# Kernel tuning notes

Measured on AMD Instinct MI355X. Metric: run time of the kernel, lower is better.

Reference implementation:

```python
import jax, jax.numpy as jnp
import numpy as np

D_MODEL = 1024
NUM_HEADS = 16
D_K = D_MODEL // NUM_HEADS


def setup_inputs() -> dict:
    key = jax.random.key(0)
    ks = jax.random.split(key, 11)
    B, S = 4, 2048
    s = 1.0 / np.sqrt(D_MODEL)
    return {
        "query": jax.random.normal(ks[0], (B, S, D_MODEL), jnp.float32),
        "key": jax.random.normal(ks[1], (B, S, D_MODEL), jnp.float32),
        "value": jax.random.normal(ks[2], (B, S, D_MODEL), jnp.float32),
        "Wq": jax.random.normal(ks[3], (D_MODEL, D_MODEL), jnp.float32) * s,
        "bq": jnp.zeros((D_MODEL,), jnp.float32),
        "Wk": jax.random.normal(ks[4], (D_MODEL, D_MODEL), jnp.float32) * s,
        "bk": jnp.zeros((D_MODEL,), jnp.float32),
        "Wv": jax.random.normal(ks[5], (D_MODEL, D_MODEL), jnp.float32) * s,
        "bv": jnp.zeros((D_MODEL,), jnp.float32),
        "Wo": jax.random.normal(ks[6], (D_MODEL, D_MODEL), jnp.float32) * s,
        "bo": jnp.zeros((D_MODEL,), jnp.float32),
    }


def reference(query, key, value, Wq, bq, Wk, bk, Wv, bv, Wo, bo):
    B, Sq, _ = query.shape
    Sk = key.shape[1]
    # linear projections (torch Linear: x @ W.T + b)
    q = query @ Wq.T + bq
    k = key @ Wk.T + bk
    v = value @ Wv.T + bv
    # [B, H, S, d_k]
    q = q.reshape(B, Sq, NUM_HEADS, D_K).transpose(0, 2, 1, 3)
    k = k.reshape(B, Sk, NUM_HEADS, D_K).transpose(0, 2, 1, 3)
    v = v.reshape(B, Sk, NUM_HEADS, D_K).transpose(0, 2, 1, 3)
    scores = jnp.einsum("bhqd,bhkd->bhqk", q, k) / jnp.sqrt(jnp.float32(D_K)).astype(q.dtype)
    attn = jax.nn.softmax(scores, axis=-1)
    out = jnp.einsum("bhqk,bhkd->bhqd", attn, v)
    out = out.transpose(0, 2, 1, 3).reshape(B, Sq, D_MODEL)
    return out @ Wo.T + bo
```

## Files before the change

kernel.cpp:

```cpp
#include <hip/hip_runtime.h>
#include <hip/hip_bf16.h>
#include <cstdint>
#include <cstddef>

typedef __attribute__((ext_vector_type(8))) short bf16x8;
typedef __attribute__((ext_vector_type(4))) short bf16x4;
typedef __attribute__((ext_vector_type(4))) float f32x4;
typedef __attribute__((ext_vector_type(2))) unsigned int u32x2;

#define NH 16
#define DK 64
#define SEQ 2048
#define DM 1024
#define QSCALE 0.18033688011112042f

__device__ __forceinline__ short f2bf(float f) {
    union { float f; unsigned u; } x; x.f = f;
    unsigned r = x.u + 0x7fffu + ((x.u >> 16) & 1u);
    return (short)(r >> 16);
}

__device__ __forceinline__ unsigned pk2(float a, float b) {
    union { float f; unsigned u; } x, y; x.f = a; y.f = b;
    return __builtin_amdgcn_perm(y.u + 0x8000u, x.u + 0x8000u, 0x07060302u);
}

__device__ __forceinline__ void glds16(const short* g, short* l) {
    __builtin_amdgcn_global_load_lds((const __attribute__((address_space(1))) unsigned int*)g,
                                     (__attribute__((address_space(3))) unsigned int*)l, 16, 0, 0);
}

__global__ __launch_bounds__(256)
void cvt_all(const float* __restrict__ xq, const float* __restrict__ xk, const float* __restrict__ xv,
             const float* __restrict__ Wq, const float* __restrict__ Wk,
             const float* __restrict__ Wv, const float* __restrict__ Wo,
             short* __restrict__ xb0, short* __restrict__ xb1, short* __restrict__ xb2,
             short* __restrict__ Wb)
{
    const int bid = blockIdx.x;
    const float* src;
    short* dst;
    float sc = 1.0f;
    int i;
    if (bid < 12288) {
        int z = bid >> 12;
        src = (z == 0) ? xq : (z == 1) ? xk : xv;
        dst = (z == 0) ? xb0 : (z == 1) ? xb1 : xb2;
        i = (bid & 4095) * 2048 + threadIdx.x * 8;
    } else {
        int wb = bid - 12288;
        int z = wb >> 9;
        src = (z == 0) ? Wq : (z == 1) ? Wk : (z == 2) ? Wv : Wo;
        dst = Wb + (size_t)z * DM * DM;
        sc = (z == 0) ? QSCALE : 1.0f;
        i = (wb & 511) * 2048 + threadIdx.x * 8;
    }
    float4 a = *(const float4*)&src[i];
    float4 b = *(const float4*)&src[i + 4];
    bf16x8 o = { f2bf(a.x * sc), f2bf(a.y * sc), f2bf(a.z * sc), f2bf(a.w * sc),
                 f2bf(b.x * sc), f2bf(b.y * sc), f2bf(b.z * sc), f2bf(b.w * sc) };
    *(bf16x8*)&dst[i] = o;
}

__global__ __launch_bounds__(256)
void cvt_x(const float* __restrict__ src, short* __restrict__ dst)
{
    int i = (blockIdx.x * 256 + threadIdx.x) * 8;
    float4 a = *(const float4*)&src[i];
    float4 b = *(const float4*)&src[i + 4];
    bf16x8 o = { f2bf(a.x), f2bf(a.y), f2bf(a.z), f2bf(a.w),
                 f2bf(b.x), f2bf(b.y), f2bf(b.z), f2bf(b.w) };
    *(bf16x8*)&dst[i] = o;
}

__global__ __launch_bounds__(256)
void cvt_w(const float* __restrict__ Wq, const float* __restrict__ Wk,
           const float* __restrict__ Wv, const float* __restrict__ Wo,
           short* __restrict__ dst)
{
    int z = blockIdx.y;
    const float* s = (z == 0) ? Wq : (z == 1) ? Wk : (z == 2) ? Wv : Wo;
    float sc = (z == 0) ? QSCALE : 1.0f;
    int i = (blockIdx.x * 256 + threadIdx.x) * 8;
    float4 a = *(const float4*)&s[i];
    float4 b = *(const float4*)&s[i + 4];
    bf16x8 o = { f2bf(a.x * sc), f2bf(a.y * sc), f2bf(a.z * sc), f2bf(a.w * sc),
                 f2bf(b.x * sc), f2bf(b.y * sc), f2bf(b.z * sc), f2bf(b.w * sc) };
    *(bf16x8*)&dst[(size_t)z * DM * DM + i] = o;
}

#define GEMM_CORE(P0, OFF0, P1, OFF1)                                                      \
    __shared__ short As[128 * 32];                                                         \
    __shared__ short Bs[128 * 32];                                                         \
    f32x4 acc[4][4] = {};                                                                  \
    const int t = threadIdx.x;                                                             \
    const int lane = t & 63;                                                               \
    const int w = t >> 6;                                                                  \
    const int wm = (w >> 1) * 64, wn = (w & 1) * 64;                                       \
    const int l15 = lane & 15, quad = lane >> 4;                                           \
    const int g0 = t, g1 = 256 + t;                                                        \
    const int r0 = g0 >> 2, r1 = g1 >> 2;                                                  \
    const int c0 = ((g0 & 3) ^ ((r0 >> 1) & 3)) * 8;                                       \
    const int c1 = ((g1 & 3) ^ ((r1 >> 1) & 3)) * 8;                                       \
    for (int k0 = 0; k0 < DM; k0 += 32) {                                                  \
        glds16(&P0[(size_t)(OFF0 + r0) * DM + k0 + c0], &As[g0 * 8]);                      \
        glds16(&P0[(size_t)(OFF0 + r1) * DM + k0 + c1], &As[g1 * 8]);                      \
        glds16(&P1[(size_t)(OFF1 + r0) * DM + k0 + c0], &Bs[g0 * 8]);                      \
        glds16(&P1[(size_t)(OFF1 + r1) * DM + k0 + c1], &Bs[g1 * 8]);                      \
        __syncthreads();                                                                   \
        bf16x8 a[4], b[4];                                                                 \
        _Pragma("unroll")                                                                  \
        for (int i = 0; i < 4; i++) {                                                      \
            int row = wm + i * 16 + l15;                                                   \
            a[i] = *(bf16x8*)&As[row * 32 + (quad ^ ((row >> 1) & 3)) * 8];                \
        }                                                                                  \
        _Pragma("unroll")                                                                  \
        for (int j = 0; j < 4; j++) {                                                      \
            int row = wn + j * 16 + l15;                                                   \
            b[j] = *(bf16x8*)&Bs[row * 32 + (quad ^ ((row >> 1) & 3)) * 8];                \
        }                                                                                  \
        _Pragma("unroll")                                                                  \
        for (int i = 0; i < 4; i++)                                                        \
            _Pragma("unroll")                                                              \
            for (int j = 0; j < 4; j++)                                                    \
                acc[i][j] = __builtin_amdgcn_mfma_f32_16x16x32_bf16(a[i], b[j], acc[i][j], 0, 0, 0); \
        __syncthreads();                                                                   \
    }

__global__ __launch_bounds__(256)
void gemm_qkv(const short* __restrict__ x0, const short* __restrict__ x1, const short* __restrict__ x2,
              const short* __restrict__ Wball,
              const float* __restrict__ bq, const float* __restrict__ bk, const float* __restrict__ bv,
              short* __restrict__ qws, short* __restrict__ kws, short* __restrict__ vws,
              int zoff)
{
    const int z = blockIdx.z + zoff;
    const short* X = (z == 0) ? x0 : (z == 1) ? x1 : x2;
    const short* W = Wball + (size_t)z * DM * DM;
    const float* bias = (z == 0) ? bq : (z == 1) ? bk : bv;
    const float bscale = (z == 0) ? QSCALE : 1.0f;

    const int tn = blockIdx.x * 128;
    const int tm = blockIdx.y * 128;
    const int vm = (z == 2);

    const short* P0 = vm ? X : W;   const int OFF0 = vm ? tm : tn;
    const short* P1 = vm ? W : X;   const int OFF1 = vm ? tn : tm;
    GEMM_CORE(P0, OFF0, P1, OFF1)

    if (vm) {
#pragma unroll
        for (int j = 0; j < 4; j++) {
            int n = tn + wn + j * 16 + l15;
            float bn = bias[n];
            int h = n >> 6, d = n & 63;
#pragma unroll
            for (int i = 0; i < 4; i++) {
                int m0 = tm + wm + i * 16 + quad * 4;
                int bb = m0 >> 11, s0 = m0 & (SEQ - 1);
                u32x2 u = { pk2(acc[i][j][0] + bn, acc[i][j][1] + bn),
                            pk2(acc[i][j][2] + bn, acc[i][j][3] + bn) };
                *(u32x2*)&vws[((size_t)((bb * NH + h) * 64 + d)) * SEQ + s0] = u;
            }
        }
    } else {
        short* dst = (z == 0) ? qws : kws;
#pragma unroll
        for (int i = 0; i < 4; i++) {
            int n0 = tn + wm + i * 16 + quad * 4;
            float4 b4 = *(const float4*)&bias[n0];
            int h = n0 >> 6, d0 = n0 & 63;
#pragma unroll
            for (int j = 0; j < 4; j++) {
                int m = tm + wn + j * 16 + l15;
                int bb = m >> 11, s = m & (SEQ - 1);
                u32x2 u = { pk2(acc[i][j][0] + b4.x * bscale, acc[i][j][1] + b4.y * bscale),
                            pk2(acc[i][j][2] + b4.z * bscale, acc[i][j][3] + b4.w * bscale) };
                *(u32x2*)&dst[((((size_t)(bb * NH + h)) * SEQ + s) << 6) + d0] = u;
            }
        }
    }
}

__global__ __launch_bounds__(256)
void out_proj(const short* __restrict__ A, const short* __restrict__ W,
              const float* __restrict__ bias, float* __restrict__ out)
{
    const int tn = blockIdx.x * 128;
    const int tm = blockIdx.y * 128;
    GEMM_CORE(A, tm, W, tn)

#pragma unroll
    for (int j = 0; j < 4; j++) {
        int n = tn + wn + j * 16 + l15;
        float bn = bias[n];
#pragma unroll
        for (int i = 0; i < 4; i++)
#pragma unroll
            for (int r = 0; r < 4; r++) {
                int m = tm + wm + i * 16 + quad * 4 + r;
                out[(size_t)m * DM + n] = acc[i][j][r] + bn;
            }
    }
}

__global__ __launch_bounds__(256, 4)
void attn(const short* __restrict__ Q, const short* __restrict__ K, const short* __restrict__ V,
          short* __restrict__ O)
{
    const int bh = blockIdx.x;
    const int b = bh >> 4, h = bh & 15;
    const int qt = blockIdx.y;
    const size_t base = (size_t)bh * SEQ * DK;
    const size_t vbase = (size_t)bh * DK * SEQ;

    const int t = threadIdx.x;
    const int lane = t & 63;
    const int w = t >> 6;
    const int l15 = lane & 15, quad = lane >> 4;
    const int l7 = l15 & 7;

    __shared__ short Kt[64 * 64];
    __shared__ short Vt[80 * 64];
    __shared__ short Pt[4][32 * 64];

    if (t < 128) {
        int row = 64 + (t >> 3);
        short val = (row == 64) ? (short)0x3F80 : (short)0;
        bf16x8 fill = { val, val, val, val, val, val, val, val };
        *(bf16x8*)&Vt[row * 64 + (t & 7) * 8] = fill;
    }

    bf16x8 qb[2][2];
    const int qrow0 = qt * 128 + w * 32;
#pragma unroll
    for (int nq = 0; nq < 2; nq++)
#pragma unroll
        for (int kd = 0; kd < 2; kd++)
            qb[nq][kd] = *(const bf16x8*)&Q[base + (size_t)(qrow0 + nq * 16 + l15) * DK + kd * 32 + quad * 8];

    f32x4 oT[5][2] = {};

    const int sr = t >> 2;
    const int sc = (t & 3) * 16;
    const int sg0 = (((t & 3) * 2) ^ (sr & 7)) * 8;
    const int sg1 = (((t & 3) * 2 + 1) ^ (sr & 7)) * 8;

    bf16x8 kr0 = *(const bf16x8*)&K[base + (size_t)sr * DK + sc];
    bf16x8 kr1 = *(const bf16x8*)&K[base + (size_t)sr * DK + sc + 8];
    bf16x8 vr0 = *(const bf16x8*)&V[vbase + (size_t)sr * SEQ + sc];
    bf16x8 vr1 = *(const bf16x8*)&V[vbase + (size_t)sr * SEQ + sc + 8];

    for (int kt = 0; kt < SEQ / 64; kt++) {
        *(bf16x8*)&Kt[sr * 64 + sg0] = kr0;
        *(bf16x8*)&Kt[sr * 64 + sg1] = kr1;
        *(bf16x8*)&Vt[sr * 64 + sg0] = vr0;
        *(bf16x8*)&Vt[sr * 64 + sg1] = vr1;
        __syncthreads();

        if (kt < SEQ / 64 - 1) {
            const short* kg = &K[base + (size_t)((kt + 1) * 64 + sr) * DK + sc];
            const short* vg = &V[vbase + (size_t)sr * SEQ + (kt + 1) * 64 + sc];
            kr0 = *(const bf16x8*)&kg[0];
            kr1 = *(const bf16x8*)&kg[8];
            vr0 = *(const bf16x8*)&vg[0];
            vr1 = *(const bf16x8*)&vg[8];
        }

        f32x4 st[4][2] = {};
#pragma unroll
        for (int kd = 0; kd < 2; kd++) {
#pragma unroll
            for (int mf = 0; mf < 4; mf++) {
                bf16x8 ka = *(bf16x8*)&Kt[(mf * 16 + l15) * 64 + ((kd * 4 + quad) ^ l7) * 8];
#pragma unroll
                for (int nq = 0; nq < 2; nq++)
                    st[mf][nq] = __builtin_amdgcn_mfma_f32_16x16x32_bf16(ka, qb[nq][kd], st[mf][nq], 0, 0, 0);
            }
        }

#pragma unroll
        for (int nq = 0; nq < 2; nq++) {
            const int prow = (nq * 16 + l15) * 64;
#pragma unroll
            for (int mf = 0; mf < 4; mf++) {
#pragma unroll
                for (int r = 0; r < 4; r++)
                    st[mf][nq][r] = __builtin_amdgcn_exp2f(st[mf][nq][r]);
                u32x2 u = { pk2(st[mf][nq][0], st[mf][nq][1]),
                            pk2(st[mf][nq][2], st[mf][nq][3]) };
                *(u32x2*)&Pt[w][prow + (((mf * 2 + (quad >> 1)) ^ l7) * 8) + (quad & 1) * 4] = u;
            }
        }

#pragma unroll
        for (int kk = 0; kk < 2; kk++) {
            bf16x8 pb[2];
#pragma unroll
            for (int nq = 0; nq < 2; nq++)
                pb[nq] = *(bf16x8*)&Pt[w][(nq * 16 + l15) * 64 + ((kk * 4 + quad) ^ l7) * 8];
#pragma unroll
            for (int mfd = 0; mfd < 5; mfd++) {
                bf16x8 va = *(bf16x8*)&Vt[(mfd * 16 + l15) * 64 + ((kk * 4 + quad) ^ l7) * 8];
#pragma unroll
                for (int nq = 0; nq < 2; nq++)
                    oT[mfd][nq] = __builtin_amdgcn_mfma_f32_16x16x32_bf16(va, pb[nq], oT[mfd][nq], 0, 0, 0);
            }
        }
        __syncthreads();
    }

#pragma unroll
    for (int nq = 0; nq < 2; nq++) {
        float lsum = __shfl(oT[4][nq][0], l15);
        float inv = 1.0f / lsum;
        int s = qrow0 + nq * 16 + l15;
#pragma unroll
        for (int mfd = 0; mfd < 4; mfd++) {
            u32x2 u = { pk2(oT[mfd][nq][0] * inv, oT[mfd][nq][1] * inv),
                        pk2(oT[mfd][nq][2] * inv, oT[mfd][nq][3] * inv) };
            *(u32x2*)&O[((size_t)(b * SEQ + s)) * DM + h * 64 + mfd * 16 + quad * 4] = u;
        }
    }
}

extern "C" void kernel_launch(void* const* d_in, const int* in_sizes, int n_in,
                              void* d_out, int out_size, void* d_ws, size_t ws_size,
                              hipStream_t stream)
{
    const float* q_in = (const float*)d_in[0];
    const float* k_in = (const float*)d_in[1];
    const float* v_in = (const float*)d_in[2];
    const float* Wq = (const float*)d_in[3];
    const float* bq = (const float*)d_in[4];
    const float* Wk = (const float*)d_in[5];
    const float* bk = (const float*)d_in[6];
    const float* Wv = (const float*)d_in[7];
    const float* bv = (const float*)d_in[8];
    const float* Wo = (const float*)d_in[9];
    const float* bo = (const float*)d_in[10];
    float* out = (float*)d_out;

    char* ws = (char*)d_ws;
    const size_t MB = (size_t)1024 * 1024;
    short* qws = (short*)d_out;
    short* kws = (short*)d_out + (size_t)8 * MB;
    const size_t NW = (size_t)DM * DM;

    if (ws_size >= 88 * MB) {
        short* xb0 = (short*)(ws);
        short* xb1 = (short*)(ws + 16 * MB);
        short* xb2 = (short*)(ws + 32 * MB);
        short* vws = (short*)(ws + 48 * MB);
        short* ows = (short*)(ws + 64 * MB);
        short* Wb  = (short*)(ws + 80 * MB);

        cvt_all<<<dim3(14336), 256, 0, stream>>>(q_in, k_in, v_in, Wq, Wk, Wv, Wo, xb0, xb1, xb2, Wb);
        gemm_qkv<<<dim3(8, 64, 3), 256, 0, stream>>>(xb0, xb1, xb2, Wb, bq, bk, bv, qws, kws, vws, 0);
        attn<<<dim3(64, 16), 256, 0, stream>>>(qws, kws, vws, ows);
        out_proj<<<dim3(8, 64), 256, 0, stream>>>(ows, Wb + 3 * NW, bo, out);
    } else {
        short* xb  = (short*)(ws);
        short* vws = (short*)(ws + 16 * MB);
        short* ows = (short*)(ws + 32 * MB);
        short* Wb  = (short*)(ws + 48 * MB);
        const int xblocks = (4 * SEQ * DM) / 2048;

        cvt_w<<<dim3((int)(NW / 2048), 4), 256, 0, stream>>>(Wq, Wk, Wv, Wo, Wb);
        cvt_x<<<dim3(xblocks), 256, 0, stream>>>(q_in, xb);
        gemm_qkv<<<dim3(8, 64, 1), 256, 0, stream>>>(xb, xb, xb, Wb, bq, bk, bv, qws, kws, vws, 0);
        cvt_x<<<dim3(xblocks), 256, 0, stream>>>(k_in, xb);
        gemm_qkv<<<dim3(8, 64, 1), 256, 0, stream>>>(xb, xb, xb, Wb, bq, bk, bv, qws, kws, vws, 1);
        cvt_x<<<dim3(xblocks), 256, 0, stream>>>(v_in, xb);
        gemm_qkv<<<dim3(8, 64, 1), 256, 0, stream>>>(xb, xb, xb, Wb, bq, bk, bv, qws, kws, vws, 2);
        attn<<<dim3(64, 16), 256, 0, stream>>>(qws, kws, vws, ows);
        out_proj<<<dim3(8, 64), 256, 0, stream>>>(ows, Wb + 3 * NW, bo, out);
    }
}
```

Baseline: 349.0 us.

## Double-buffer LDS tiles in GEMM and attention with async global-to-LDS loads

Both the projection GEMM core and the attention loop now use two LDS buffers. The next tile is issued while the current one is computed, so only one barrier is needed per tile. In attention, the register-staged K/V prefetch is replaced with direct global-to-LDS loads into ping-pong buffers, and the V ones-row fill is set up in both buffers. The aim is to hide global memory latency behind MFMA work. The cost is doubled LDS use, which lowers occupancy; the attention launch bound drops from 4 to 3 blocks per CU to match.

```diff
diff --git a/kernel.cpp b/kernel.cpp
--- a/kernel.cpp
+++ b/kernel.cpp
@@ -89,10 +89,38 @@
     *(bf16x8*)&dst[(size_t)z * DM * DM + i] = o;
 }
 
+#define GEMM_STAGE(Adst, Bdst, kk)                                                         \
+    glds16(&P0_[(size_t)(OFF0_ + r0) * DM + (kk) + c0], &Adst[g0 * 8]);                    \
+    glds16(&P0_[(size_t)(OFF0_ + r1) * DM + (kk) + c1], &Adst[g1 * 8]);                    \
+    glds16(&P1_[(size_t)(OFF1_ + r0) * DM + (kk) + c0], &Bdst[g0 * 8]);                    \
+    glds16(&P1_[(size_t)(OFF1_ + r1) * DM + (kk) + c1], &Bdst[g1 * 8]);
+
+#define GEMM_TILE(Asrc, Bsrc)                                                              \
+    {                                                                                      \
+        bf16x8 a[4], b[4];                                                                 \
+        _Pragma("unroll")                                                                  \
+        for (int i = 0; i < 4; i++) {                                                      \
+            int row = wm + i * 16 + l15;                                                   \
+            a[i] = *(bf16x8*)&Asrc[row * 32 + (quad ^ ((row >> 1) & 3)) * 8];              \
+        }                                                                                  \
+        _Pragma("unroll")                                                                  \
+        for (int j = 0; j < 4; j++) {                                                      \
+            int row = wn + j * 16 + l15;                                                   \
+            b[j] = *(bf16x8*)&Bsrc[row * 32 + (quad ^ ((row >> 1) & 3)) * 8];              \
+        }                                                                                  \
+        _Pragma("unroll")                                                                  \
+        for (int i = 0; i < 4; i++)                                                        \
+            _Pragma("unroll")                                                              \
+            for (int j = 0; j < 4; j++)                                                    \
+                acc[i][j] = __builtin_amdgcn_mfma_f32_16x16x32_bf16(a[i], b[j], acc[i][j], 0, 0, 0); \
+    }
+
 #define GEMM_CORE(P0, OFF0, P1, OFF1)                                                      \
-    __shared__ short As[128 * 32];                                                         \
-    __shared__ short Bs[128 * 32];                                                         \
+    __shared__ short As0[128 * 32], As1[128 * 32];                                         \
+    __shared__ short Bs0[128 * 32], Bs1[128 * 32];                                         \
     f32x4 acc[4][4] = {};                                                                  \
+    const short* P0_ = (P0);  const int OFF0_ = (OFF0);                                    \
+    const short* P1_ = (P1);  const int OFF1_ = (OFF1);                                    \
     const int t = threadIdx.x;                                                             \
     const int lane = t & 63;                                                               \
     const int w = t >> 6;                                                                  \
@@ -102,29 +130,14 @@
     const int r0 = g0 >> 2, r1 = g1 >> 2;                                                  \
     const int c0 = ((g0 & 3) ^ ((r0 >> 1) & 3)) * 8;                                       \
     const int c1 = ((g1 & 3) ^ ((r1 >> 1) & 3)) * 8;                                       \
-    for (int k0 = 0; k0 < DM; k0 += 32) {                                                  \
-        glds16(&P0[(size_t)(OFF0 + r0) * DM + k0 + c0], &As[g0 * 8]);                      \
-        glds16(&P0[(size_t)(OFF0 + r1) * DM + k0 + c1], &As[g1 * 8]);                      \
-        glds16(&P1[(size_t)(OFF1 + r0) * DM + k0 + c0], &Bs[g0 * 8]);                      \
-        glds16(&P1[(size_t)(OFF1 + r1) * DM + k0 + c1], &Bs[g1 * 8]);                      \
+    GEMM_STAGE(As0, Bs0, 0)                                                                \
+    for (int k0 = 0; k0 < DM; k0 += 64) {                                                  \
         __syncthreads();                                                                   \
-        bf16x8 a[4], b[4];                                                                 \
-        _Pragma("unroll")                                                                  \
-        for (int i = 0; i < 4; i++) {                                                      \
-            int row = wm + i * 16 + l15;                                                   \
-            a[i] = *(bf16x8*)&As[row * 32 + (quad ^ ((row >> 1) & 3)) * 8];                \
-        }                                                                                  \
-        _Pragma("unroll")                                                                  \
-        for (int j = 0; j < 4; j++) {                                                      \
-            int row = wn + j * 16 + l15;                                                   \
-            b[j] = *(bf16x8*)&Bs[row * 32 + (quad ^ ((row >> 1) & 3)) * 8];                \
-        }                                                                                  \
-        _Pragma("unroll")                                                                  \
-        for (int i = 0; i < 4; i++)                                                        \
-            _Pragma("unroll")                                                              \
-            for (int j = 0; j < 4; j++)                                                    \
-                acc[i][j] = __builtin_amdgcn_mfma_f32_16x16x32_bf16(a[i], b[j], acc[i][j], 0, 0, 0); \
+        GEMM_STAGE(As1, Bs1, k0 + 32)                                                      \
+        GEMM_TILE(As0, Bs0)                                                                \
         __syncthreads();                                                                   \
+        if (k0 + 64 < DM) { GEMM_STAGE(As0, Bs0, k0 + 64) }                                \
+        GEMM_TILE(As1, Bs1)                                                                \
     }
 
 __global__ __launch_bounds__(256)
@@ -144,9 +157,7 @@
     const int tm = blockIdx.y * 128;
     const int vm = (z == 2);
 
-    const short* P0 = vm ? X : W;   const int OFF0 = vm ? tm : tn;
-    const short* P1 = vm ? W : X;   const int OFF1 = vm ? tn : tm;
-    GEMM_CORE(P0, OFF0, P1, OFF1)
+    GEMM_CORE(vm ? X : W, vm ? tm : tn, vm ? W : X, vm ? tn : tm)
 
     if (vm) {
 #pragma unroll
@@ -204,7 +215,55 @@
     }
 }
 
-__global__ __launch_bounds__(256, 4)
+#define ATTN_STAGE(kt, Kdst, Vdst)                                                         \
+    glds16(&K[base + (size_t)((kt) * 64 + rA) * DK + kcA], &Kdst[gA * 8]);                 \
+    glds16(&K[base + (size_t)((kt) * 64 + rB) * DK + kcB], &Kdst[gB * 8]);                 \
+    glds16(&V[vbase + (size_t)rA * SEQ + (kt) * 64 + kcA], &Vdst[gA * 8]);                 \
+    glds16(&V[vbase + (size_t)rB * SEQ + (kt) * 64 + kcB], &Vdst[gB * 8]);
+
+#define ATTN_TILE(KB, VB)                                                                  \
+    {                                                                                      \
+        f32x4 st[4][2] = {};                                                               \
+        _Pragma("unroll")                                                                  \
+        for (int kd = 0; kd < 2; kd++) {                                                   \
+            _Pragma("unroll")                                                              \
+            for (int mf = 0; mf < 4; mf++) {                                               \
+                bf16x8 ka = *(bf16x8*)&KB[(mf * 16 + l15) * 64 + ((kd * 4 + quad) ^ l7) * 8]; \
+                _Pragma("unroll")                                                          \
+                for (int nq = 0; nq < 2; nq++)                                             \
+                    st[mf][nq] = __builtin_amdgcn_mfma_f32_16x16x32_bf16(ka, qb[nq][kd], st[mf][nq], 0, 0, 0); \
+            }                                                                              \
+        }                                                                                  \
+        _Pragma("unroll")                                                                  \
+        for (int nq = 0; nq < 2; nq++) {                                                   \
+            const int prow = (nq * 16 + l15) * 64;                                         \
+            _Pragma("unroll")                                                              \
+            for (int mf = 0; mf < 4; mf++) {                                               \
+                _Pragma("unroll")                                                          \
+                for (int r = 0; r < 4; r++)                                                \
+                    st[mf][nq][r] = __builtin_amdgcn_exp2f(st[mf][nq][r]);                 \
+                u32x2 u = { pk2(st[mf][nq][0], st[mf][nq][1]),                             \
+                            pk2(st[mf][nq][2], st[mf][nq][3]) };                           \
+                *(u32x2*)&Pt[w][prow + (((mf * 2 + (quad >> 1)) ^ l7) * 8) + (quad & 1) * 4] = u; \
+            }                                                                              \
+        }                                                                                  \
+        _Pragma("unroll")                                                                  \
+        for (int kk = 0; kk < 2; kk++) {                                                   \
+            bf16x8 pb[2];                                                                  \
+            _Pragma("unroll")                                                              \
+            for (int nq = 0; nq < 2; nq++)                                                 \
+                pb[nq] = *(bf16x8*)&Pt[w][(nq * 16 + l15) * 64 + ((kk * 4 + quad) ^ l7) * 8]; \
+            _Pragma("unroll")                                                              \
+            for (int mfd = 0; mfd < 5; mfd++) {                                            \
+                bf16x8 va = *(bf16x8*)&VB[(mfd * 16 + l15) * 64 + ((kk * 4 + quad) ^ l7) * 8]; \
+                _Pragma("unroll")                                                          \
+                for (int nq = 0; nq < 2; nq++)                                             \
+                    oT[mfd][nq] = __builtin_amdgcn_mfma_f32_16x16x32_bf16(va, pb[nq], oT[mfd][nq], 0, 0, 0); \
+            }                                                                              \
+        }                                                                                  \
+    }
+
+__global__ __launch_bounds__(256, 3)
 void attn(const short* __restrict__ Q, const short* __restrict__ K, const short* __restrict__ V,
           short* __restrict__ O)
 {
@@ -220,16 +279,22 @@
     const int l15 = lane & 15, quad = lane >> 4;
     const int l7 = l15 & 7;
 
-    __shared__ short Kt[64 * 64];
-    __shared__ short Vt[80 * 64];
+    __shared__ short Kt0[64 * 64], Kt1[64 * 64];
+    __shared__ short Vt0[80 * 64], Vt1[80 * 64];
     __shared__ short Pt[4][32 * 64];
 
-    if (t < 128) {
-        int row = 64 + (t >> 3);
-        short val = (row == 64) ? (short)0x3F80 : (short)0;
+    {
+        int rrow = (t >> 3) & 15;
+        short val = (rrow == 0) ? (short)0x3F80 : (short)0;
         bf16x8 fill = { val, val, val, val, val, val, val, val };
-        *(bf16x8*)&Vt[row * 64 + (t & 7) * 8] = fill;
-    }
+        short* Vx = (t < 128) ? Vt0 : Vt1;
+        *(bf16x8*)&Vx[(64 + rrow) * 64 + (t & 7) * 8] = fill;
+    }
+
+    const int gA = t, gB = t + 256;
+    const int rA = gA >> 3, rB = gB >> 3;
+    const int kcA = ((gA & 7) ^ (rA & 7)) * 8;
+    const int kcB = ((gB & 7) ^ (rB & 7)) * 8;
 
     bf16x8 qb[2][2];
     const int qrow0 = qt * 128 + w * 32;
@@ -241,73 +306,14 @@
 
     f32x4 oT[5][2] = {};
 
-    const int sr = t >> 2;
-    const int sc = (t & 3) * 16;
-    const int sg0 = (((t & 3) * 2) ^ (sr & 7)) * 8;
-    const int sg1 = (((t & 3) * 2 + 1) ^ (sr & 7)) * 8;
-
-    bf16x8 kr0 = *(const bf16x8*)&K[base + (size_t)sr * DK + sc];
-    bf16x8 kr1 = *(const bf16x8*)&K[base + (size_t)sr * DK + sc + 8];
-    bf16x8 vr0 = *(const bf16x8*)&V[vbase + (size_t)sr * SEQ + sc];
-    bf16x8 vr1 = *(const bf16x8*)&V[vbase + (size_t)sr * SEQ + sc + 8];
-
-    for (int kt = 0; kt < SEQ / 64; kt++) {
-        *(bf16x8*)&Kt[sr * 64 + sg0] = kr0;
-        *(bf16x8*)&Kt[sr * 64 + sg1] = kr1;
-        *(bf16x8*)&Vt[sr * 64 + sg0] = vr0;
-        *(bf16x8*)&Vt[sr * 64 + sg1] = vr1;
+    ATTN_STAGE(0, Kt0, Vt0)
+    for (int kt = 0; kt < SEQ / 64; kt += 2) {
         __syncthreads();
-
-        if (kt < SEQ / 64 - 1) {
-            const short* kg = &K[base + (size_t)((kt + 1) * 64 + sr) * DK + sc];
-            const short* vg = &V[vbase + (size_t)sr * SEQ + (kt + 1) * 64 + sc];
-            kr0 = *(const bf16x8*)&kg[0];
-            kr1 = *(const bf16x8*)&kg[8];
-            vr0 = *(const bf16x8*)&vg[0];
-            vr1 = *(const bf16x8*)&vg[8];
-        }
-
-        f32x4 st[4][2] = {};
-#pragma unroll
-        for (int kd = 0; kd < 2; kd++) {
-#pragma unroll
-            for (int mf = 0; mf < 4; mf++) {
-                bf16x8 ka = *(bf16x8*)&Kt[(mf * 16 + l15) * 64 + ((kd * 4 + quad) ^ l7) * 8];
-#pragma unroll
-                for (int nq = 0; nq < 2; nq++)
-                    st[mf][nq] = __builtin_amdgcn_mfma_f32_16x16x32_bf16(ka, qb[nq][kd], st[mf][nq], 0, 0, 0);
-            }
-        }
-
-#pragma unroll
-        for (int nq = 0; nq < 2; nq++) {
-            const int prow = (nq * 16 + l15) * 64;
-#pragma unroll
-            for (int mf = 0; mf < 4; mf++) {
-#pragma unroll
-                for (int r = 0; r < 4; r++)
-                    st[mf][nq][r] = __builtin_amdgcn_exp2f(st[mf][nq][r]);
-                u32x2 u = { pk2(st[mf][nq][0], st[mf][nq][1]),
-                            pk2(st[mf][nq][2], st[mf][nq][3]) };
-                *(u32x2*)&Pt[w][prow + (((mf * 2 + (quad >> 1)) ^ l7) * 8) + (quad & 1) * 4] = u;
-            }
-        }
-
-#pragma unroll
-        for (int kk = 0; kk < 2; kk++) {
-            bf16x8 pb[2];
-#pragma unroll
-            for (int nq = 0; nq < 2; nq++)
-                pb[nq] = *(bf16x8*)&Pt[w][(nq * 16 + l15) * 64 + ((kk * 4 + quad) ^ l7) * 8];
-#pragma unroll
-            for (int mfd = 0; mfd < 5; mfd++) {
-                bf16x8 va = *(bf16x8*)&Vt[(mfd * 16 + l15) * 64 + ((kk * 4 + quad) ^ l7) * 8];
-#pragma unroll
-                for (int nq = 0; nq < 2; nq++)
-                    oT[mfd][nq] = __builtin_amdgcn_mfma_f32_16x16x32_bf16(va, pb[nq], oT[mfd][nq], 0, 0, 0);
-            }
-        }
+        ATTN_STAGE(kt + 1, Kt1, Vt1)
+        ATTN_TILE(Kt0, Vt0)
         __syncthreads();
+        if (kt + 2 < SEQ / 64) { ATTN_STAGE(kt + 2, Kt0, Vt0) }
+        ATTN_TILE(Kt1, Vt1)
     }
 
 #pragma unroll
```

New measurement: 349.5 us. Within noise of the previous version (+0.1%).
